# Kernel optimization log

Hardware: AMD Instinct MI355X
Metric: run time of the kernel (lower is better)

## Reference

```python
import jax, jax.numpy as jnp
import numpy as np

N = 100000
E = 1600000
D = 128
EPS = 1e-5


def setup_inputs() -> dict:
    key = jax.random.key(0)
    ks = jax.random.split(key, 8)
    s = 1.0 / np.sqrt(D)
    feats = jax.random.normal(ks[0], (N, D), dtype=jnp.float32)
    src = jax.random.randint(ks[1], (E,), 0, N, dtype=jnp.int32)
    dst = jax.random.randint(ks[2], (E,), 0, N, dtype=jnp.int32)
    W_gcn = jax.random.normal(ks[3], (D, D), dtype=jnp.float32) * s
    b_gcn = jnp.zeros((D,), dtype=jnp.float32)
    W_res = jax.random.normal(ks[4], (D, D), dtype=jnp.float32) * s
    b_res = jnp.zeros((D,), dtype=jnp.float32)
    g1 = jnp.ones((D,), dtype=jnp.float32)
    be1 = jnp.zeros((D,), dtype=jnp.float32)
    g2 = jnp.ones((D,), dtype=jnp.float32)
    be2 = jnp.zeros((D,), dtype=jnp.float32)
    return {"feats": feats, "W_gcn": W_gcn, "b_gcn": b_gcn, "W_res": W_res,
            "b_res": b_res, "g1": g1, "be1": be1, "g2": g2, "be2": be2,
            "src": src, "dst": dst}


def _batchnorm(x, gamma, beta):
    # BatchNorm1d, training mode: biased batch stats over the node dim
    mu = jnp.mean(x, axis=0)
    var = jnp.var(x, axis=0)
    return gamma * (x - mu) * jax.lax.rsqrt(var + EPS) + beta


def reference(feats, W_gcn, b_gcn, W_res, b_res, g1, be1, g2, be2, src, dst):
    n = feats.shape[0]
    # GraphConv(norm='none'): sum-aggregate neighbor feats then linear (in<=out)
    agg = jax.ops.segment_sum(feats[src], dst, num_segments=n)  # [N, D]
    h = jax.nn.relu(agg @ W_gcn + b_gcn)
    # dgllife GCNLayer internal residual: activation(Linear(feats))
    res = jax.nn.relu(feats @ W_res + b_res)
    h = _batchnorm(h + res, g1, be1)
    # outer ResidualGCNLayer: Identity residual (in_feats==out_feats) + BN
    out = _batchnorm(h + feats, g2, be2)
    return out
```

## Files before the change

kernel.cpp:

```cpp
#include <hip/hip_runtime.h>
#include <hip/hip_bf16.h>
#include <stdint.h>

#define NN 100000
#define EE 1600000
#define DD 128
#define EPSV 1e-5f
#define WWIN 128
#define NB 782
#define NCLS 8
#define NSEG (NB * NCLS)
#define ITEMS (EE / 4)
#define ITEMS_PER_CLS (ITEMS / NCLS)
#define SORTCAP 4096

typedef __attribute__((ext_vector_type(8))) short short8;
typedef __attribute__((ext_vector_type(4))) float floatx4;
typedef unsigned short u16;

union S8 { short8 v; short s[8]; unsigned short u[8]; };

__device__ __forceinline__ float bf2f(u16 u) {
    return __uint_as_float(((unsigned int)u) << 16);
}
__device__ __forceinline__ u16 f2bf(float f) {
    unsigned int x = __float_as_uint(f);
    x += 0x7FFFu + ((x >> 16) & 1u);
    return (u16)(x >> 16);
}


__global__ void k_detect(const float* __restrict__ f, int* __restrict__ flag) {
    __shared__ int cnt;
    if (threadIdx.x == 0) cnt = 0;
    __syncthreads();
    const float v = fabsf(f[threadIdx.x]);
    if (v > 1e-3f && v < 1e3f) atomicAdd(&cnt, 1);
    __syncthreads();
    if (threadIdx.x == 0) *flag = (cnt >= 128) ? 1 : 0;
}

__global__ __launch_bounds__(256) void k_convert_feats(
    const int* __restrict__ flag, const float* __restrict__ ff,
    u16* __restrict__ fc)
{
    if (*flag == 0) return;
    const size_t P = (size_t)NN * (DD / 2);
    for (size_t i = (size_t)blockIdx.x * blockDim.x + threadIdx.x; i < P;
         i += (size_t)gridDim.x * blockDim.x) {
        const float2 v = *(const float2*)(ff + 2 * i);
        const unsigned int o = (unsigned int)f2bf(v.x) | ((unsigned int)f2bf(v.y) << 16);
        *(unsigned int*)(fc + 2 * i) = o;
    }
}

__global__ __launch_bounds__(256) void k_convert_params(
    const int* __restrict__ flag,
    const float* __restrict__ Wg, const float* __restrict__ Wr,
    const float* __restrict__ bg, const float* __restrict__ br,
    const float* __restrict__ g1, const float* __restrict__ g2,
    const float* __restrict__ be2, u16* __restrict__ pc)
{
    if (*flag == 0) return;
    const int i = blockIdx.x * blockDim.x + threadIdx.x;
    if (i >= 33408) return;
    float v;
    if (i < 16384)      v = Wg[i];
    else if (i < 32768) v = Wr[i - 16384];
    else {
        const int j = i - 32768;
        const int a = j >> 7, o = j & 127;
        v = (a == 0) ? bg[o] : (a == 1) ? br[o] : (a == 2) ? g1[o]
          : (a == 3) ? g2[o] : be2[o];
    }
    pc[i] = f2bf(v);
}

__global__ __launch_bounds__(256) void k_hist2(
    const int* __restrict__ dst, int* __restrict__ cnt)
{
    __shared__ int lc[NB];
    const int cls  = blockIdx.x & 7;
    const int blk  = blockIdx.x >> 3;
    const int nblk = gridDim.x >> 3;
    const int it0  = cls * ITEMS_PER_CLS;
    const int it1  = it0 + ITEMS_PER_CLS;
    for (int i = threadIdx.x; i < NB; i += 256) lc[i] = 0;
    __syncthreads();
    const int4* __restrict__ dst4 = (const int4*)dst;
    for (int it = it0 + blk * blockDim.x + threadIdx.x; it < it1;
         it += nblk * blockDim.x) {
        const int4 d = dst4[it];
        atomicAdd(&lc[d.x >> 7], 1);
        atomicAdd(&lc[d.y >> 7], 1);
        atomicAdd(&lc[d.z >> 7], 1);
        atomicAdd(&lc[d.w >> 7], 1);
    }
    __syncthreads();
    for (int i = threadIdx.x; i < NB; i += 256) {
        const int v = lc[i];
        if (v) atomicAdd(&cnt[i * NCLS + cls], v);
    }
}

__global__ __launch_bounds__(1024) void k_scanseg(
    const int* __restrict__ cnt, int* __restrict__ off,
    int* __restrict__ cursor)
{
    const int tx = threadIdx.x;
    const int lane = tx & 63, w = tx >> 6;
    __shared__ int wsum[16];
    __shared__ int carry;
    if (tx == 0) carry = 0;
    __syncthreads();
    for (int base = 0; base < NSEG; base += 1024) {
        const int i = base + tx;
        const int v = (i < NSEG) ? cnt[i] : 0;
        int incl = v;
#pragma unroll
        for (int d = 1; d < 64; d <<= 1) {
            const int n = __shfl_up(incl, d, 64);
            if (lane >= d) incl += n;
        }
        if (lane == 63) wsum[w] = incl;
        __syncthreads();
        if (tx < 16) {
            int s = wsum[tx];
#pragma unroll
            for (int d = 1; d < 16; d <<= 1) {
                const int n = __shfl_up(s, d, 16);
                if ((tx & 15) >= d) s += n;
            }
            wsum[tx] = s;
        }
        __syncthreads();
        const int c = carry;
        const int woff = (w == 0) ? 0 : wsum[w - 1];
        if (i < NSEG) {
            const int excl = c + woff + incl - v;
            off[i] = excl;
            cursor[i] = excl;
        }
        __syncthreads();
        if (tx == 0) carry = c + wsum[15];
        __syncthreads();
    }
    if (tx == 0) off[NSEG] = carry;
}

__global__ __launch_bounds__(256) void k_bin(
    const int* __restrict__ src, const int* __restrict__ dst,
    int* __restrict__ cursor, unsigned int* __restrict__ arena)
{
    __shared__ int lc[NB], lb[NB];
    const int cls  = blockIdx.x & 7;
    const int blk  = blockIdx.x >> 3;
    const int nblk = gridDim.x >> 3;
    const int it0  = cls * ITEMS_PER_CLS;
    const int it1  = it0 + ITEMS_PER_CLS;
    const int4* __restrict__ dst4 = (const int4*)dst;
    const int4* __restrict__ src4 = (const int4*)src;
    for (int i = threadIdx.x; i < NB; i += 256) lc[i] = 0;
    __syncthreads();
    for (int it = it0 + blk * blockDim.x + threadIdx.x; it < it1;
         it += nblk * blockDim.x) {
        const int4 d = dst4[it];
        atomicAdd(&lc[d.x >> 7], 1);
        atomicAdd(&lc[d.y >> 7], 1);
        atomicAdd(&lc[d.z >> 7], 1);
        atomicAdd(&lc[d.w >> 7], 1);
    }
    __syncthreads();
    for (int i = threadIdx.x; i < NB; i += 256) {
        const int v = lc[i];
        lb[i] = v ? atomicAdd(&cursor[i * NCLS + cls], v) : 0;
    }
    __syncthreads();
    for (int i = threadIdx.x; i < NB; i += 256) lc[i] = 0;
    __syncthreads();
    for (int it = it0 + blk * blockDim.x + threadIdx.x; it < it1;
         it += nblk * blockDim.x) {
        const int4 d = dst4[it];
        const int4 s = src4[it];
        int wv, p;
        wv = d.x >> 7; p = lb[wv] + atomicAdd(&lc[wv], 1);
        arena[p] = ((unsigned int)(d.x & 127) << 17) | (unsigned int)s.x;
        wv = d.y >> 7; p = lb[wv] + atomicAdd(&lc[wv], 1);
        arena[p] = ((unsigned int)(d.y & 127) << 17) | (unsigned int)s.y;
        wv = d.z >> 7; p = lb[wv] + atomicAdd(&lc[wv], 1);
        arena[p] = ((unsigned int)(d.z & 127) << 17) | (unsigned int)s.z;
        wv = d.w >> 7; p = lb[wv] + atomicAdd(&lc[wv], 1);
        arena[p] = ((unsigned int)(d.w & 127) << 17) | (unsigned int)s.w;
    }
}

__global__ __launch_bounds__(256) void k_winsort(
    unsigned int* __restrict__ arena, const int* __restrict__ off,
    int* __restrict__ row_st)
{
    __shared__ unsigned int buf[SORTCAP];
    __shared__ int cnt[WWIN], pref[WWIN], cur[WWIN];
    const int tx = threadIdx.x;
    const int b = blockIdx.x;
    const int s0 = off[b * NCLS];
    const int s1 = off[b * NCLS + NCLS];
    int len = s1 - s0;
    if (len > SORTCAP) len = SORTCAP;
    if (tx < WWIN) cnt[tx] = 0;
    __syncthreads();
    for (int i = tx; i < len; i += 256) {
        const unsigned int p = arena[s0 + i];
        buf[i] = p;
        atomicAdd(&cnt[p >> 17], 1);
    }
    __syncthreads();
    if (tx < WWIN) pref[tx] = cnt[tx];
    __syncthreads();
    for (int d = 1; d < WWIN; d <<= 1) {
        int v = 0;
        if (tx < WWIN && tx >= d) v = pref[tx - d];
        __syncthreads();
        if (tx < WWIN) pref[tx] += v;
        __syncthreads();
    }
    if (tx < WWIN) {
        const int excl = pref[tx] - cnt[tx];
        cur[tx] = excl;
        const int node = b * WWIN + tx;
        if (node < NN) row_st[node] = s0 + excl;
    }
    if (b == NB - 1 && tx == 0) row_st[NN] = EE;
    __syncthreads();
    for (int i = tx; i < len; i += 256) {
        const unsigned int p = buf[i];
        const int pos = atomicAdd(&cur[p >> 17], 1);
        arena[s0 + pos] = p & 0x1FFFFu;
    }
}

__global__ __launch_bounds__(256, 8) void k_gather(
    const int* __restrict__ flag,
    const u16* __restrict__ feats_raw, const u16* __restrict__ feats_c,
    const int* __restrict__ edge_s, const int* __restrict__ row_st,
    u16* __restrict__ aggb)
{
    const u16* __restrict__ F = (*flag != 0) ? feats_c : feats_raw;
    const int lane = threadIdx.x & 63;
    const int l16  = lane & 15;
    const int gb   = lane & 48;
    const int wave = (blockIdx.x * blockDim.x + threadIdx.x) >> 6;
    const int nw   = (gridDim.x * blockDim.x) >> 6;

    for (int n0 = wave * 4; n0 < NN; n0 += nw * 4) {
        const int node = n0 + (lane >> 4);
        const int rs   = row_st[node];
        const int deg  = row_st[node + 1] - rs;
        float a0 = 0.f, a1 = 0.f, a2 = 0.f, a3 = 0.f;
        float a4 = 0.f, a5 = 0.f, a6 = 0.f, a7 = 0.f;
        for (int ebase = 0; ebase < deg; ebase += 16) {
            const int rem = deg - ebase;
            const int nb  = rem < 16 ? rem : 16;
            int il = 0;
            if (l16 < nb) il = edge_s[rs + ebase + l16];
            int j = 0;
            for (; j + 8 <= nb; j += 8) {
                uint4 vv[8];
#pragma unroll
                for (int q = 0; q < 8; ++q) {
                    const int s = __shfl(il, gb + j + q, 64);
                    vv[q] = *(const uint4*)(F + (size_t)s * DD + l16 * 8);
                }
#pragma unroll
                for (int q = 0; q < 8; ++q) {
                    a0 += bf2f((u16)(vv[q].x & 0xFFFFu));
                    a1 += bf2f((u16)(vv[q].x >> 16));
                    a2 += bf2f((u16)(vv[q].y & 0xFFFFu));
                    a3 += bf2f((u16)(vv[q].y >> 16));
                    a4 += bf2f((u16)(vv[q].z & 0xFFFFu));
                    a5 += bf2f((u16)(vv[q].z >> 16));
                    a6 += bf2f((u16)(vv[q].w & 0xFFFFu));
                    a7 += bf2f((u16)(vv[q].w >> 16));
                }
            }
            for (; j + 4 <= nb; j += 4) {
                uint4 vv[4];
#pragma unroll
                for (int q = 0; q < 4; ++q) {
                    const int s = __shfl(il, gb + j + q, 64);
                    vv[q] = *(const uint4*)(F + (size_t)s * DD + l16 * 8);
                }
#pragma unroll
                for (int q = 0; q < 4; ++q) {
                    a0 += bf2f((u16)(vv[q].x & 0xFFFFu));
                    a1 += bf2f((u16)(vv[q].x >> 16));
                    a2 += bf2f((u16)(vv[q].y & 0xFFFFu));
                    a3 += bf2f((u16)(vv[q].y >> 16));
                    a4 += bf2f((u16)(vv[q].z & 0xFFFFu));
                    a5 += bf2f((u16)(vv[q].z >> 16));
                    a6 += bf2f((u16)(vv[q].w & 0xFFFFu));
                    a7 += bf2f((u16)(vv[q].w >> 16));
                }
            }
            for (; j < nb; ++j) {
                const int s = __shfl(il, gb + j, 64);
                const uint4 v = *(const uint4*)(F + (size_t)s * DD + l16 * 8);
                a0 += bf2f((u16)(v.x & 0xFFFFu));
                a1 += bf2f((u16)(v.x >> 16));
                a2 += bf2f((u16)(v.y & 0xFFFFu));
                a3 += bf2f((u16)(v.y >> 16));
                a4 += bf2f((u16)(v.z & 0xFFFFu));
                a5 += bf2f((u16)(v.z >> 16));
                a6 += bf2f((u16)(v.w & 0xFFFFu));
                a7 += bf2f((u16)(v.w >> 16));
            }
        }
        uint4 o;
        o.x = (unsigned int)f2bf(a0) | ((unsigned int)f2bf(a1) << 16);
        o.y = (unsigned int)f2bf(a2) | ((unsigned int)f2bf(a3) << 16);
        o.z = (unsigned int)f2bf(a4) | ((unsigned int)f2bf(a5) << 16);
        o.w = (unsigned int)f2bf(a6) | ((unsigned int)f2bf(a7) << 16);
        *(uint4*)(aggb + (size_t)node * DD + l16 * 8) = o;
    }
}

__global__ __launch_bounds__(256) void k_gemm(
    const int* __restrict__ flag,
    const u16* __restrict__ aggb,
    const u16* __restrict__ feats_raw, const u16* __restrict__ feats_c,
    const u16* __restrict__ Wg_raw, const u16* __restrict__ bg_raw,
    const u16* __restrict__ Wr_raw, const u16* __restrict__ br_raw,
    const u16* __restrict__ pc,
    u16* __restrict__ t_out)
{
    const bool f32 = (*flag != 0);
    const u16* __restrict__ F  = f32 ? feats_c     : feats_raw;
    const u16* __restrict__ Wg = f32 ? pc          : Wg_raw;
    const u16* __restrict__ Wr = f32 ? pc + 16384  : Wr_raw;
    const u16* __restrict__ bg = f32 ? pc + 32768  : bg_raw;
    const u16* __restrict__ br = f32 ? pc + 32896  : br_raw;

    const int lane = threadIdx.x & 63;
    const int wv   = threadIdx.x >> 6;
    const int l15  = lane & 15;
    const int quad = lane >> 4;
    const int c0 = wv * 16 + l15;
    const int c1 = 64 + wv * 16 + l15;

    S8 fg0[4], fg1[4], fr0[4], fr1[4];
#pragma unroll
    for (int kb = 0; kb < 4; ++kb) {
        const int kr = kb * 32 + quad * 8;
#pragma unroll
        for (int j = 0; j < 8; ++j) {
            fg0[kb].u[j] = Wg[(size_t)(kr + j) * DD + c0];
            fg1[kb].u[j] = Wg[(size_t)(kr + j) * DD + c1];
            fr0[kb].u[j] = Wr[(size_t)(kr + j) * DD + c0];
            fr1[kb].u[j] = Wr[(size_t)(kr + j) * DD + c1];
        }
    }
    const float bgc0 = bf2f(bg[c0]), bgc1 = bf2f(bg[c1]);
    const float brc0 = bf2f(br[c0]), brc1 = bf2f(br[c1]);

    for (int tile = blockIdx.x; tile < NN / 16; tile += gridDim.x) {
        const int row0 = tile * 16;
        const int arow = row0 + l15;
        floatx4 ag0 = {0.f,0.f,0.f,0.f}, ag1 = {0.f,0.f,0.f,0.f};
        floatx4 ar0 = {0.f,0.f,0.f,0.f}, ar1 = {0.f,0.f,0.f,0.f};
#pragma unroll
        for (int kb = 0; kb < 4; ++kb) {
            const int kbase = kb * 32 + quad * 8;
            S8 av, ff;
            av.v = *(const short8*)(aggb + (size_t)arow * DD + kbase);
            ff.v = *(const short8*)(F    + (size_t)arow * DD + kbase);
            ag0 = __builtin_amdgcn_mfma_f32_16x16x32_bf16(av.v, fg0[kb].v, ag0, 0, 0, 0);
            ag1 = __builtin_amdgcn_mfma_f32_16x16x32_bf16(av.v, fg1[kb].v, ag1, 0, 0, 0);
            ar0 = __builtin_amdgcn_mfma_f32_16x16x32_bf16(ff.v, fr0[kb].v, ar0, 0, 0, 0);
            ar1 = __builtin_amdgcn_mfma_f32_16x16x32_bf16(ff.v, fr1[kb].v, ar1, 0, 0, 0);
        }
#pragma unroll
        for (int r = 0; r < 4; ++r) {
            const int row = row0 + quad * 4 + r;
            const float t0 = fmaxf(ag0[r] + bgc0, 0.f) + fmaxf(ar0[r] + brc0, 0.f);
            const float t1 = fmaxf(ag1[r] + bgc1, 0.f) + fmaxf(ar1[r] + brc1, 0.f);
            t_out[(size_t)row * DD + c0] = f2bf(t0);
            t_out[(size_t)row * DD + c1] = f2bf(t1);
        }
    }
}

__global__ __launch_bounds__(256) void k_stats(
    const int* __restrict__ flag,
    const u16* __restrict__ t,
    const u16* __restrict__ feats_raw, const u16* __restrict__ feats_c,
    float* __restrict__ stats)
{
    const u16* __restrict__ F = (*flag != 0) ? feats_c : feats_raw;
    const int tx = threadIdx.x;
    const int c2 = (tx & 63) * 2;
    const int rg = tx >> 6;
    float acc[10];
#pragma unroll
    for (int k = 0; k < 10; ++k) acc[k] = 0.f;

    for (int r = blockIdx.x * 4 + rg; r < NN; r += gridDim.x * 4) {
        const unsigned int tv = *(const unsigned int*)(t + (size_t)r * DD + c2);
        const unsigned int fv = *(const unsigned int*)(F + (size_t)r * DD + c2);
        const float t0 = bf2f((u16)(tv & 0xFFFFu));
        const float t1 = bf2f((u16)(tv >> 16));
        const float f0 = bf2f((u16)(fv & 0xFFFFu));
        const float f1 = bf2f((u16)(fv >> 16));
        acc[0] += t0;      acc[1] += t1;
        acc[2] += t0 * t0; acc[3] += t1 * t1;
        acc[4] += f0;      acc[5] += f1;
        acc[6] += f0 * f0; acc[7] += f1 * f1;
        acc[8] += t0 * f0; acc[9] += t1 * f1;
    }

    __shared__ float red[256][10];
#pragma unroll
    for (int k = 0; k < 10; ++k) red[tx][k] = acc[k];
    __syncthreads();
    if (tx < 64) {
#pragma unroll
        for (int k = 0; k < 10; ++k) {
            const float v = red[tx][k] + red[tx + 64][k] + red[tx + 128][k] + red[tx + 192][k];
            unsafeAtomicAdd(&stats[(k >> 1) * DD + c2 + (k & 1)], v);
        }
    }
}

__global__ __launch_bounds__(256) void k_final(
    const int* __restrict__ flag,
    const u16* __restrict__ t,
    const u16* __restrict__ feats_raw, const u16* __restrict__ feats_c,
    const u16* __restrict__ g1_raw, const u16* __restrict__ g2_raw,
    const u16* __restrict__ be2_raw, const u16* __restrict__ pc,
    const float* __restrict__ stats,
    void* __restrict__ out)
{
    const bool f32 = (*flag != 0);
    const u16* __restrict__ F   = f32 ? feats_c    : feats_raw;
    const u16* __restrict__ g1  = f32 ? pc + 33024 : g1_raw;
    const u16* __restrict__ g2  = f32 ? pc + 33152 : g2_raw;
    const u16* __restrict__ be2 = f32 ? pc + 33280 : be2_raw;

    __shared__ float sA[DD], sB[DD], sG[DD];
    if (threadIdx.x < DD) {
        const int c = threadIdx.x;
        const float invN = 1.0f / (float)NN;
        const float St  = stats[c],          Stt = stats[DD + c];
        const float Sf  = stats[2 * DD + c], Sff = stats[3 * DD + c];
        const float Stf = stats[4 * DD + c];
        const float mu1  = St * invN;
        const float vart = fmaxf(Stt * invN - mu1 * mu1, 0.f);
        const float muf  = Sf * invN;
        const float varf = fmaxf(Sff * invN - muf * muf, 0.f);
        const float cov  = Stf * invN - mu1 * muf;
        const float r1   = rsqrtf(vart + EPSV);
        const float a1   = bf2f(g1[c]) * r1;
        const float var2 = fmaxf(a1 * a1 * vart + 2.f * a1 * cov + varf, 0.f);
        const float r2   = rsqrtf(var2 + EPSV);
        const float g2r2 = bf2f(g2[c]) * r2;
        sA[c] = g2r2 * a1;
        sB[c] = g2r2;
        sG[c] = bf2f(be2[c]) - g2r2 * (a1 * mu1 + muf);
    }
    __syncthreads();

    float* outf = (float*)out;
    u16*   outb = (u16*)out;
    const size_t P = (size_t)NN * (DD / 2);
    for (size_t i = (size_t)blockIdx.x * blockDim.x + threadIdx.x; i < P;
         i += (size_t)gridDim.x * blockDim.x) {
        const int c = ((int)(i & 63)) * 2;
        const unsigned int tv = *(const unsigned int*)(t + 2 * i);
        const unsigned int fv = *(const unsigned int*)(F + 2 * i);
        const float o0 = sA[c]     * bf2f((u16)(tv & 0xFFFFu))
                       + sB[c]     * bf2f((u16)(fv & 0xFFFFu)) + sG[c];
        const float o1 = sA[c + 1] * bf2f((u16)(tv >> 16))
                       + sB[c + 1] * bf2f((u16)(fv >> 16)) + sG[c + 1];
        if (f32) {
            float2 o; o.x = o0; o.y = o1;
            *(float2*)(outf + 2 * i) = o;
        } else {
            const unsigned int ov = (unsigned int)f2bf(o0) | ((unsigned int)f2bf(o1) << 16);
            *(unsigned int*)(outb + 2 * i) = ov;
        }
    }
}

extern "C" void kernel_launch(void* const* d_in, const int* in_sizes, int n_in,
                              void* d_out, int out_size, void* d_ws, size_t ws_size,
                              hipStream_t stream) {
    const u16* feats = (const u16*)d_in[0];
    const u16* Wg    = (const u16*)d_in[1];
    const u16* bg    = (const u16*)d_in[2];
    const u16* Wr    = (const u16*)d_in[3];
    const u16* br    = (const u16*)d_in[4];
    const u16* g1    = (const u16*)d_in[5];
    const u16* g2    = (const u16*)d_in[7];
    const u16* be2   = (const u16*)d_in[8];
    const int* src = (const int*)d_in[9];
    const int* dst = (const int*)d_in[10];

    char* ws = (char*)d_ws;
    u16*          aggb    = (u16*)  ws;
    u16*          t       = (u16*)  (ws + 25600000);
    u16*          feats_c = (u16*)  (ws + 51200000);
    u16*          pc      = (u16*)  (ws + 76800000);
    float*        stats   = (float*)(ws + 76866816);
    int*          flag    = (int*)  (ws + 76869376);
    int*          cnt     = (int*)  (ws + 76869632);
    int*          off     = (int*)  (ws + 76894656);
    int*          cursor  = (int*)  (ws + 76919684);
    int*          row_st  = (int*)  (ws + 76944708);
    unsigned int* arena   = (unsigned int*)(ws + 77344712);

    hipMemsetAsync(cnt,   0, NSEG * sizeof(int), stream);
    hipMemsetAsync(stats, 0, 5 * DD * sizeof(float), stream);

    k_detect<<<1, 256, 0, stream>>>((const float*)d_in[0], flag);
    k_convert_feats<<<1024, 256, 0, stream>>>(flag, (const float*)d_in[0], feats_c);
    k_convert_params<<<131, 256, 0, stream>>>(flag,
        (const float*)d_in[1], (const float*)d_in[3], (const float*)d_in[2],
        (const float*)d_in[4], (const float*)d_in[5], (const float*)d_in[7],
        (const float*)d_in[8], pc);

    k_hist2  <<<256, 256, 0, stream>>>(dst, cnt);
    k_scanseg<<<1, 1024, 0, stream>>>(cnt, off, cursor);
    k_bin    <<<256, 256, 0, stream>>>(src, dst, cursor, arena);
    k_winsort<<<NB, 256, 0, stream>>>(arena, off, row_st);

    k_gather<<<2048, 256, 0, stream>>>(flag, feats, feats_c, (const int*)arena, row_st, aggb);
    k_gemm  <<<1024, 256, 0, stream>>>(flag, aggb, feats, feats_c, Wg, bg, Wr, br, pc, t);
    k_stats <<<784,  256, 0, stream>>>(flag, t, feats, feats_c, stats);
    k_final <<<2048, 256, 0, stream>>>(flag, t, feats, feats_c, g1, g2, be2, pc, stats, d_out);
}
```

Baseline: 341.6 us.

## Fuse BN statistics into GEMM epilogue, merge convert kernels, widen final loads

Drops the separate stats kernel: the GEMM epilogue now accumulates per-column sum, sum of squares and cross products of t and feats, reduces them across the wave with shuffles, and adds them to the stats buffer atomically. The two conversion kernels become one launch, and the feature conversion and final output pass now move four elements per thread instead of two. The aim is to avoid re-reading t and feats from memory and to cut launch count, at the cost of extra scalar feats loads and more atomics in the GEMM epilogue.

```diff
diff --git a/kernel.cpp b/kernel.cpp
--- a/kernel.cpp
+++ b/kernel.cpp
@@ -40,40 +40,41 @@
     if (threadIdx.x == 0) *flag = (cnt >= 128) ? 1 : 0;
 }
 
-__global__ __launch_bounds__(256) void k_convert_feats(
+__global__ __launch_bounds__(256) void k_convert(
     const int* __restrict__ flag, const float* __restrict__ ff,
-    u16* __restrict__ fc)
-{
-    if (*flag == 0) return;
-    const size_t P = (size_t)NN * (DD / 2);
-    for (size_t i = (size_t)blockIdx.x * blockDim.x + threadIdx.x; i < P;
-         i += (size_t)gridDim.x * blockDim.x) {
-        const float2 v = *(const float2*)(ff + 2 * i);
-        const unsigned int o = (unsigned int)f2bf(v.x) | ((unsigned int)f2bf(v.y) << 16);
-        *(unsigned int*)(fc + 2 * i) = o;
-    }
-}
-
-__global__ __launch_bounds__(256) void k_convert_params(
-    const int* __restrict__ flag,
     const float* __restrict__ Wg, const float* __restrict__ Wr,
     const float* __restrict__ bg, const float* __restrict__ br,
     const float* __restrict__ g1, const float* __restrict__ g2,
-    const float* __restrict__ be2, u16* __restrict__ pc)
+    const float* __restrict__ be2,
+    u16* __restrict__ fc, u16* __restrict__ pc)
 {
     if (*flag == 0) return;
-    const int i = blockIdx.x * blockDim.x + threadIdx.x;
-    if (i >= 33408) return;
-    float v;
-    if (i < 16384)      v = Wg[i];
-    else if (i < 32768) v = Wr[i - 16384];
-    else {
-        const int j = i - 32768;
-        const int a = j >> 7, o = j & 127;
-        v = (a == 0) ? bg[o] : (a == 1) ? br[o] : (a == 2) ? g1[o]
-          : (a == 3) ? g2[o] : be2[o];
-    }
-    pc[i] = f2bf(v);
+    const int bx = blockIdx.x;
+    if (bx < 131) {
+        const int i = bx * 256 + threadIdx.x;
+        if (i >= 33408) return;
+        float v;
+        if (i < 16384)      v = Wg[i];
+        else if (i < 32768) v = Wr[i - 16384];
+        else {
+            const int j = i - 32768;
+            const int a = j >> 7, o = j & 127;
+            v = (a == 0) ? bg[o] : (a == 1) ? br[o] : (a == 2) ? g1[o]
+              : (a == 3) ? g2[o] : be2[o];
+        }
+        pc[i] = f2bf(v);
+        return;
+    }
+    const int bid = bx - 131;
+    const size_t P = (size_t)NN * (DD / 4);
+    for (size_t i = (size_t)bid * 256 + threadIdx.x; i < P;
+         i += (size_t)1024 * 256) {
+        const float4 v = *(const float4*)(ff + 4 * i);
+        uint2 o;
+        o.x = (unsigned int)f2bf(v.x) | ((unsigned int)f2bf(v.y) << 16);
+        o.y = (unsigned int)f2bf(v.z) | ((unsigned int)f2bf(v.w) << 16);
+        *(uint2*)(fc + 4 * i) = o;
+    }
 }
 
 __global__ __launch_bounds__(256) void k_hist2(
@@ -330,7 +331,7 @@
     const u16* __restrict__ Wg_raw, const u16* __restrict__ bg_raw,
     const u16* __restrict__ Wr_raw, const u16* __restrict__ br_raw,
     const u16* __restrict__ pc,
-    u16* __restrict__ t_out)
+    u16* __restrict__ t_out, float* __restrict__ stats)
 {
     const bool f32 = (*flag != 0);
     const u16* __restrict__ F  = f32 ? feats_c     : feats_raw;
@@ -360,6 +361,10 @@
     }
     const float bgc0 = bf2f(bg[c0]), bgc1 = bf2f(bg[c1]);
     const float brc0 = bf2f(br[c0]), brc1 = bf2f(br[c1]);
+
+    float s_t0 = 0.f, s_t1 = 0.f, s_tt0 = 0.f, s_tt1 = 0.f;
+    float s_f0 = 0.f, s_f1 = 0.f, s_ff0 = 0.f, s_ff1 = 0.f;
+    float s_tf0 = 0.f, s_tf1 = 0.f;
 
     for (int tile = blockIdx.x; tile < NN / 16; tile += gridDim.x) {
         const int row0 = tile * 16;
@@ -380,52 +385,37 @@
 #pragma unroll
         for (int r = 0; r < 4; ++r) {
             const int row = row0 + quad * 4 + r;
-            const float t0 = fmaxf(ag0[r] + bgc0, 0.f) + fmaxf(ar0[r] + brc0, 0.f);
-            const float t1 = fmaxf(ag1[r] + bgc1, 0.f) + fmaxf(ar1[r] + brc1, 0.f);
-            t_out[(size_t)row * DD + c0] = f2bf(t0);
-            t_out[(size_t)row * DD + c1] = f2bf(t1);
-        }
-    }
-}
-
-__global__ __launch_bounds__(256) void k_stats(
-    const int* __restrict__ flag,
-    const u16* __restrict__ t,
-    const u16* __restrict__ feats_raw, const u16* __restrict__ feats_c,
-    float* __restrict__ stats)
-{
-    const u16* __restrict__ F = (*flag != 0) ? feats_c : feats_raw;
-    const int tx = threadIdx.x;
-    const int c2 = (tx & 63) * 2;
-    const int rg = tx >> 6;
-    float acc[10];
-#pragma unroll
-    for (int k = 0; k < 10; ++k) acc[k] = 0.f;
-
-    for (int r = blockIdx.x * 4 + rg; r < NN; r += gridDim.x * 4) {
-        const unsigned int tv = *(const unsigned int*)(t + (size_t)r * DD + c2);
-        const unsigned int fv = *(const unsigned int*)(F + (size_t)r * DD + c2);
-        const float t0 = bf2f((u16)(tv & 0xFFFFu));
-        const float t1 = bf2f((u16)(tv >> 16));
-        const float f0 = bf2f((u16)(fv & 0xFFFFu));
-        const float f1 = bf2f((u16)(fv >> 16));
-        acc[0] += t0;      acc[1] += t1;
-        acc[2] += t0 * t0; acc[3] += t1 * t1;
-        acc[4] += f0;      acc[5] += f1;
-        acc[6] += f0 * f0; acc[7] += f1 * f1;
-        acc[8] += t0 * f0; acc[9] += t1 * f1;
-    }
-
-    __shared__ float red[256][10];
-#pragma unroll
-    for (int k = 0; k < 10; ++k) red[tx][k] = acc[k];
-    __syncthreads();
-    if (tx < 64) {
-#pragma unroll
-        for (int k = 0; k < 10; ++k) {
-            const float v = red[tx][k] + red[tx + 64][k] + red[tx + 128][k] + red[tx + 192][k];
-            unsafeAtomicAdd(&stats[(k >> 1) * DD + c2 + (k & 1)], v);
-        }
+            const u16 tb0 = f2bf(fmaxf(ag0[r] + bgc0, 0.f) + fmaxf(ar0[r] + brc0, 0.f));
+            const u16 tb1 = f2bf(fmaxf(ag1[r] + bgc1, 0.f) + fmaxf(ar1[r] + brc1, 0.f));
+            t_out[(size_t)row * DD + c0] = tb0;
+            t_out[(size_t)row * DD + c1] = tb1;
+            const float t0 = bf2f(tb0), t1 = bf2f(tb1);
+            const float fv0 = bf2f(F[(size_t)row * DD + c0]);
+            const float fv1 = bf2f(F[(size_t)row * DD + c1]);
+            s_t0  += t0;        s_t1  += t1;
+            s_tt0 += t0 * t0;   s_tt1 += t1 * t1;
+            s_f0  += fv0;       s_f1  += fv1;
+            s_ff0 += fv0 * fv0; s_ff1 += fv1 * fv1;
+            s_tf0 += t0 * fv0;  s_tf1 += t1 * fv1;
+        }
+    }
+
+#define QRED(x) x += __shfl_xor(x, 16, 64); x += __shfl_xor(x, 32, 64);
+    QRED(s_t0)  QRED(s_t1)  QRED(s_tt0) QRED(s_tt1)
+    QRED(s_f0)  QRED(s_f1)  QRED(s_ff0) QRED(s_ff1)
+    QRED(s_tf0) QRED(s_tf1)
+#undef QRED
+    if (quad == 0) {
+        unsafeAtomicAdd(&stats[0 * DD + c0], s_t0);
+        unsafeAtomicAdd(&stats[0 * DD + c1], s_t1);
+        unsafeAtomicAdd(&stats[1 * DD + c0], s_tt0);
+        unsafeAtomicAdd(&stats[1 * DD + c1], s_tt1);
+        unsafeAtomicAdd(&stats[2 * DD + c0], s_f0);
+        unsafeAtomicAdd(&stats[2 * DD + c1], s_f1);
+        unsafeAtomicAdd(&stats[3 * DD + c0], s_ff0);
+        unsafeAtomicAdd(&stats[3 * DD + c1], s_ff1);
+        unsafeAtomicAdd(&stats[4 * DD + c0], s_tf0);
+        unsafeAtomicAdd(&stats[4 * DD + c1], s_tf1);
     }
 }
 
@@ -469,22 +459,28 @@
 
     float* outf = (float*)out;
     u16*   outb = (u16*)out;
-    const size_t P = (size_t)NN * (DD / 2);
+    const size_t P = (size_t)NN * (DD / 4);
     for (size_t i = (size_t)blockIdx.x * blockDim.x + threadIdx.x; i < P;
          i += (size_t)gridDim.x * blockDim.x) {
-        const int c = ((int)(i & 63)) * 2;
-        const unsigned int tv = *(const unsigned int*)(t + 2 * i);
-        const unsigned int fv = *(const unsigned int*)(F + 2 * i);
-        const float o0 = sA[c]     * bf2f((u16)(tv & 0xFFFFu))
-                       + sB[c]     * bf2f((u16)(fv & 0xFFFFu)) + sG[c];
-        const float o1 = sA[c + 1] * bf2f((u16)(tv >> 16))
-                       + sB[c + 1] * bf2f((u16)(fv >> 16)) + sG[c + 1];
+        const int c = ((int)(i & 31)) * 4;
+        const uint2 tv = *(const uint2*)(t + 4 * i);
+        const uint2 fv = *(const uint2*)(F + 4 * i);
+        const float o0 = sA[c]     * bf2f((u16)(tv.x & 0xFFFFu))
+                       + sB[c]     * bf2f((u16)(fv.x & 0xFFFFu)) + sG[c];
+        const float o1 = sA[c + 1] * bf2f((u16)(tv.x >> 16))
+                       + sB[c + 1] * bf2f((u16)(fv.x >> 16)) + sG[c + 1];
+        const float o2 = sA[c + 2] * bf2f((u16)(tv.y & 0xFFFFu))
+                       + sB[c + 2] * bf2f((u16)(fv.y & 0xFFFFu)) + sG[c + 2];
+        const float o3 = sA[c + 3] * bf2f((u16)(tv.y >> 16))
+                       + sB[c + 3] * bf2f((u16)(fv.y >> 16)) + sG[c + 3];
         if (f32) {
-            float2 o; o.x = o0; o.y = o1;
-            *(float2*)(outf + 2 * i) = o;
+            float4 o; o.x = o0; o.y = o1; o.z = o2; o.w = o3;
+            *(float4*)(outf + 4 * i) = o;
         } else {
-            const unsigned int ov = (unsigned int)f2bf(o0) | ((unsigned int)f2bf(o1) << 16);
-            *(unsigned int*)(outb + 2 * i) = ov;
+            uint2 ov;
+            ov.x = (unsigned int)f2bf(o0) | ((unsigned int)f2bf(o1) << 16);
+            ov.y = (unsigned int)f2bf(o2) | ((unsigned int)f2bf(o3) << 16);
+            *(uint2*)(outb + 4 * i) = ov;
         }
     }
 }
@@ -520,11 +516,10 @@
     hipMemsetAsync(stats, 0, 5 * DD * sizeof(float), stream);
 
     k_detect<<<1, 256, 0, stream>>>((const float*)d_in[0], flag);
-    k_convert_feats<<<1024, 256, 0, stream>>>(flag, (const float*)d_in[0], feats_c);
-    k_convert_params<<<131, 256, 0, stream>>>(flag,
+    k_convert<<<1155, 256, 0, stream>>>(flag, (const float*)d_in[0],
         (const float*)d_in[1], (const float*)d_in[3], (const float*)d_in[2],
         (const float*)d_in[4], (const float*)d_in[5], (const float*)d_in[7],
-        (const float*)d_in[8], pc);
+        (const float*)d_in[8], feats_c, pc);
 
     k_hist2  <<<256, 256, 0, stream>>>(dst, cnt);
     k_scanseg<<<1, 1024, 0, stream>>>(cnt, off, cursor);
@@ -532,7 +527,6 @@
     k_winsort<<<NB, 256, 0, stream>>>(arena, off, row_st);
 
     k_gather<<<2048, 256, 0, stream>>>(flag, feats, feats_c, (const int*)arena, row_st, aggb);
-    k_gemm  <<<1024, 256, 0, stream>>>(flag, aggb, feats, feats_c, Wg, bg, Wr, br, pc, t);
-    k_stats <<<784,  256, 0, stream>>>(flag, t, feats, feats_c, stats);
+    k_gemm  <<<1024, 256, 0, stream>>>(flag, aggb, feats, feats_c, Wg, bg, Wr, br, pc, t, stats);
     k_final <<<2048, 256, 0, stream>>>(flag, t, feats, feats_c, g1, g2, be2, pc, stats, d_out);
 }
```

Result: faster. 305.1 us (-10.7%).
